# Kernel optimization log

Hardware: AMD Instinct MI355X
Metric: run time of the kernel (lower is better)

The kernel has to match this reference:

```python
import jax, jax.numpy as jnp
import numpy as np

B, N, C, H, T = 64, 4096, 768, 12, 10


def setup_inputs() -> dict:
    key = jax.random.key(0)
    kx, kq, kk, kv, kp = jax.random.split(key, 5)
    std = 0.02  # trunc_normal std from _init_weights
    return {
        "x": jax.random.normal(kx, (B, N, C), jnp.float32),
        "Wq": std * jax.random.normal(kq, (C, C), jnp.float32),
        "Wk": std * jax.random.normal(kk, (C, C), jnp.float32),
        "Wv": std * jax.random.normal(kv, (C, C), jnp.float32),
        "Wp": std * jax.random.normal(kp, (C, C), jnp.float32),
        "bp": jnp.zeros((C,), jnp.float32),
        "nb_task_tokens": T,
    }


def reference(x, Wq, Wk, Wv, Wp, bp, nb_task_tokens):
    Bq, Nq, Cq = x.shape
    d = Cq // H
    scale = d ** -0.5
    Tt = nb_task_tokens
    # q only from the first T (task) tokens; k, v from all N tokens
    q = (x[:, :Tt] @ Wq).reshape(Bq, Tt, H, d).transpose(0, 2, 1, 3) * scale  # [B,H,T,d]
    k = (x @ Wk).reshape(Bq, Nq, H, d).transpose(0, 2, 1, 3)                  # [B,H,N,d]
    v = (x @ Wv).reshape(Bq, Nq, H, d).transpose(0, 2, 1, 3)                  # [B,H,N,d]
    attn = jnp.einsum("bhtd,bhnd->bhtn", q, k)                                # [B,H,T,N]
    # mask: task token i may attend to itself and to all patch tokens (cols >= T),
    # but not to other task tokens
    rows = jnp.arange(Tt)[:, None]
    cols = jnp.arange(Nq)[None, :]
    allowed = (cols >= Tt) | (cols == rows)                                   # [T,N]
    attn = jnp.where(allowed, attn, -jnp.inf)
    attn = jax.nn.softmax(attn, axis=-1)
    x_cls = jnp.einsum("bhtn,bhnd->bhtd", attn, v)                            # [B,H,T,d]
    x_cls = x_cls.transpose(0, 2, 1, 3).reshape(Bq, Tt, Cq)
    x_cls = x_cls @ Wp + bp
    return (x_cls, attn, v)
```

## Files before the change

### kernel.cpp

```cpp
#include <hip/hip_runtime.h>

typedef __attribute__((ext_vector_type(8))) short short8;
typedef __attribute__((ext_vector_type(4))) short short4v;
typedef __attribute__((ext_vector_type(4))) float f32x4;

__device__ __forceinline__ unsigned short f2bf(float f) {
  union { float f; unsigned u; } v; v.f = f;
  unsigned r = v.u + 0x7FFFu + ((v.u >> 16) & 1u);
  return (unsigned short)(r >> 16);
}

__device__ __forceinline__ float bf2f(unsigned short h) {
  union { unsigned u; float f; } v; v.u = ((unsigned)h) << 16;
  return v.f;
}

__device__ __forceinline__ void gload16(const void* g, void* l) {
  __builtin_amdgcn_global_load_lds(
      (const __attribute__((address_space(1))) void*)g,
      (__attribute__((address_space(3))) void*)l, 16, 0, 0);
}

__global__ __launch_bounds__(256) void conv_x(const float* __restrict__ x,
                                              unsigned short* __restrict__ xb) {
  const long total = 25165824;
  long stride = (long)gridDim.x * 256;
  for (long u = blockIdx.x * 256 + threadIdx.x; u < total; u += stride) {
    const float* p = x + u * 8;
    float4 a = *(const float4*)p;
    float4 b = *(const float4*)(p + 4);
    short8 h;
    h[0] = (short)f2bf(a.x); h[1] = (short)f2bf(a.y);
    h[2] = (short)f2bf(a.z); h[3] = (short)f2bf(a.w);
    h[4] = (short)f2bf(b.x); h[5] = (short)f2bf(b.y);
    h[6] = (short)f2bf(b.z); h[7] = (short)f2bf(b.w);
    *(short8*)(xb + u * 8) = h;
  }
}

__global__ __launch_bounds__(256) void prep_w(const float* __restrict__ Wk,
                                              const float* __restrict__ Wv,
                                              unsigned short* __restrict__ Wt) {
  int idx = blockIdx.x * 256 + threadIdx.x;
  int n = idx / 768, k = idx - n * 768;
  float w = (n < 768) ? Wk[k * 768 + n] : Wv[k * 768 + (n - 768)];
  Wt[idx] = f2bf(w);
}

__global__ __launch_bounds__(256) void q_proj(const float* __restrict__ x,
                                              const float* __restrict__ Wq,
                                              unsigned short* __restrict__ q_ws) {
  int b = blockIdx.x, tid = threadIdx.x;
  __shared__ float xr[7680];
  const float* xp = x + (long)b * 4096 * 768;
  for (int i = tid; i < 7680; i += 256) xr[i] = xp[i];
  for (int i = tid; i < 12 * 6 * 64; i += 256) {
    int h = i / 384, rem = i - h * 384;
    int t = 10 + rem / 64, d = rem & 63;
    q_ws[(((long)(b * 12 + h) * 16 + t) << 6) + d] = 0;
  }
  __syncthreads();
  float acc[10][3];
#pragma unroll
  for (int t = 0; t < 10; ++t) { acc[t][0] = 0.f; acc[t][1] = 0.f; acc[t][2] = 0.f; }
  for (int k = 0; k < 768; ++k) {
    const float* wr = Wq + (long)k * 768;
    float w0 = wr[tid], w1 = wr[tid + 256], w2 = wr[tid + 512];
#pragma unroll
    for (int t = 0; t < 10; ++t) {
      float xv = xr[t * 768 + k];
      acc[t][0] += xv * w0; acc[t][1] += xv * w1; acc[t][2] += xv * w2;
    }
  }
#pragma unroll
  for (int t = 0; t < 10; ++t) {
#pragma unroll
    for (int j = 0; j < 3; ++j) {
      int c = tid + j * 256;
      int h = c >> 6, d = c & 63;
      q_ws[(((long)(b * 12 + h) * 16 + t) << 6) + d] = f2bf(acc[t][j] * 0.125f);
    }
  }
}

__global__ __launch_bounds__(512, 2) void gemm_kv8(const unsigned short* __restrict__ xb,
                                                   const unsigned short* __restrict__ Wt,
                                                   unsigned short* __restrict__ k_ws,
                                                   float* __restrict__ v_out) {
  __shared__ char smem[131072];
#define A0T ((unsigned short*)(smem))
#define B0T ((unsigned short*)(smem + 32768))
#define A1T ((unsigned short*)(smem + 65536))
#define B1T ((unsigned short*)(smem + 98304))

  int bid = blockIdx.x;
  int lb = (bid & 7) * 768 + (bid >> 3);
  int mt = lb / 6, nt = lb - mt * 6;
  long m0 = (long)mt * 256; int n0 = nt * 256;
  int tid = threadIdx.x, lane = tid & 63;
  int uw = __builtin_amdgcn_readfirstlane(tid >> 6);
  int wm = uw >> 2, wn = uw & 3;
  int r16 = lane & 15, gk = lane >> 4;

  const unsigned short* xs = xb + m0 * 768;
  const unsigned short* wp = Wt + (long)n0 * 768;

  int srow8 = lane >> 3;
  int sch = ((lane & 7) ^ (srow8 & 7)) << 3;
  const unsigned short* sA = xs + (long)(uw * 8 + srow8) * 768 + sch;
  const unsigned short* sB = wp + (long)(uw * 8 + srow8) * 768 + sch;

  int ck0 = ((gk ^ (r16 & 7)) << 3);
  int ck1 = (((4 + gk) ^ (r16 & 7)) << 3);
  int arb = (wm * 128 + r16) * 64;
  int brb = (wn * 64 + r16) * 64;

  f32x4 acc[8][4];
#pragma unroll
  for (int i = 0; i < 8; ++i)
#pragma unroll
    for (int j = 0; j < 4; ++j) acc[i][j] = (f32x4){0.f, 0.f, 0.f, 0.f};

#define SGA(AT, I, KO) gload16(sA + (long)(I) * 49152 + (KO), (AT) + ((I) * 64 + uw * 8) * 64)
#define SGB(BT, I, KO) gload16(sB + (long)(I) * 49152 + (KO), (BT) + ((I) * 64 + uw * 8) * 64)
#define WBND asm volatile("s_waitcnt vmcnt(0)\n\ts_barrier" ::: "memory")
#define PBAR __builtin_amdgcn_s_barrier()

#define BODY(AC, BC, AN, BN, KOS, DOST)                                         \
  {                                                                             \
    short8 fa[4][2], fb0[2][2], fb1[2][2];                                      \
    if (DOST) { SGA(AN, 0, KOS); SGA(AN, 1, KOS); SGB(BN, 0, KOS); SGB(BN, 1, KOS); } \
    _Pragma("unroll")                                                           \
    for (int mi = 0; mi < 4; ++mi) {                                            \
      fa[mi][0] = *(const short8*)&AC[arb + mi * 1024 + ck0];                   \
      fa[mi][1] = *(const short8*)&AC[arb + mi * 1024 + ck1];                   \
    }                                                                           \
    _Pragma("unroll")                                                           \
    for (int ni = 0; ni < 2; ++ni) {                                            \
      fb0[ni][0] = *(const short8*)&BC[brb + ni * 1024 + ck0];                  \
      fb0[ni][1] = *(const short8*)&BC[brb + ni * 1024 + ck1];                  \
    }                                                                           \
    PBAR;                                                                       \
    __builtin_amdgcn_s_setprio(1);                                              \
    _Pragma("unroll")                                                           \
    for (int mi = 0; mi < 4; ++mi)                                              \
      _Pragma("unroll")                                                         \
      for (int ni = 0; ni < 2; ++ni) {                                          \
        acc[mi][ni] = __builtin_amdgcn_mfma_f32_16x16x32_bf16(fa[mi][0], fb0[ni][0], acc[mi][ni], 0, 0, 0); \
        acc[mi][ni] = __builtin_amdgcn_mfma_f32_16x16x32_bf16(fa[mi][1], fb0[ni][1], acc[mi][ni], 0, 0, 0); \
      }                                                                         \
    __builtin_amdgcn_s_setprio(0);                                              \
    PBAR;                                                                       \
    if (DOST) { SGA(AN, 2, KOS); SGA(AN, 3, KOS); SGB(BN, 2, KOS); SGB(BN, 3, KOS); } \
    _Pragma("unroll")                                                           \
    for (int ni = 0; ni < 2; ++ni) {                                            \
      fb1[ni][0] = *(const short8*)&BC[brb + (ni + 2) * 1024 + ck0];            \
      fb1[ni][1] = *(const short8*)&BC[brb + (ni + 2) * 1024 + ck1];            \
    }                                                                           \
    PBAR;                                                                       \
    __builtin_amdgcn_s_setprio(1);                                              \
    _Pragma("unroll")                                                           \
    for (int mi = 0; mi < 4; ++mi)                                              \
      _Pragma("unroll")                                                         \
      for (int ni = 0; ni < 2; ++ni) {                                          \
        acc[mi][ni + 2] = __builtin_amdgcn_mfma_f32_16x16x32_bf16(fa[mi][0], fb1[ni][0], acc[mi][ni + 2], 0, 0, 0); \
        acc[mi][ni + 2] = __builtin_amdgcn_mfma_f32_16x16x32_bf16(fa[mi][1], fb1[ni][1], acc[mi][ni + 2], 0, 0, 0); \
      }                                                                         \
    __builtin_amdgcn_s_setprio(0);                                              \
    PBAR;                                                                       \
    _Pragma("unroll")                                                           \
    for (int mi = 0; mi < 4; ++mi) {                                            \
      fa[mi][0] = *(const short8*)&AC[arb + (mi + 4) * 1024 + ck0];             \
      fa[mi][1] = *(const short8*)&AC[arb + (mi + 4) * 1024 + ck1];             \
    }                                                                           \
    PBAR;                                                                       \
    __builtin_amdgcn_s_setprio(1);                                              \
    _Pragma("unroll")                                                           \
    for (int mi = 0; mi < 4; ++mi)                                              \
      _Pragma("unroll")                                                         \
      for (int ni = 0; ni < 2; ++ni) {                                          \
        acc[mi + 4][ni + 2] = __builtin_amdgcn_mfma_f32_16x16x32_bf16(fa[mi][0], fb1[ni][0], acc[mi + 4][ni + 2], 0, 0, 0); \
        acc[mi + 4][ni + 2] = __builtin_amdgcn_mfma_f32_16x16x32_bf16(fa[mi][1], fb1[ni][1], acc[mi + 4][ni + 2], 0, 0, 0); \
      }                                                                         \
    __builtin_amdgcn_s_setprio(0);                                              \
    PBAR;                                                                       \
    __builtin_amdgcn_s_setprio(1);                                              \
    _Pragma("unroll")                                                           \
    for (int mi = 0; mi < 4; ++mi)                                              \
      _Pragma("unroll")                                                         \
      for (int ni = 0; ni < 2; ++ni) {                                          \
        acc[mi + 4][ni] = __builtin_amdgcn_mfma_f32_16x16x32_bf16(fa[mi][0], fb0[ni][0], acc[mi + 4][ni], 0, 0, 0); \
        acc[mi + 4][ni] = __builtin_amdgcn_mfma_f32_16x16x32_bf16(fa[mi][1], fb0[ni][1], acc[mi + 4][ni], 0, 0, 0); \
      }                                                                         \
    __builtin_amdgcn_s_setprio(0);                                              \
  }

  SGA(A0T, 0, 0); SGA(A0T, 1, 0); SGA(A0T, 2, 0); SGA(A0T, 3, 0);
  SGB(B0T, 0, 0); SGB(B0T, 1, 0); SGB(B0T, 2, 0); SGB(B0T, 3, 0);
  WBND;

#pragma unroll 1
  for (int t = 0; t < 12; t += 2) {
    BODY(A0T, B0T, A1T, B1T, (t + 1) * 64, true);
    WBND;
    BODY(A1T, B1T, A0T, B0T, (t + 2) * 64, (t + 2) < 12);
    WBND;
  }
#undef BODY
#undef SGA
#undef SGB
#undef WBND
#undef PBAR

  float* scr = (float*)smem + uw * 1088;
  bool is_k = (n0 < 768);
  int h = (is_k ? (n0 >> 6) : ((n0 - 768) >> 6)) + wn;
  int bq = (int)(m0 >> 12);
  int nb = (int)(m0 & 4095) + wm * 128;

#pragma unroll
  for (int mi = 0; mi < 8; ++mi) {
#pragma unroll
    for (int ni = 0; ni < 4; ++ni)
#pragma unroll
      for (int r = 0; r < 4; ++r)
        scr[(gk * 4 + r) * 68 + ni * 16 + r16] = acc[mi][ni][r];
    int nbase = nb + mi * 16;
    if (is_k) {
#pragma unroll
      for (int p = 0; p < 2; ++p) {
        int row = p * 8 + (lane >> 3), d0 = (lane & 7) << 3;
        float4 aa = *(const float4*)&scr[row * 68 + d0];
        float4 bb = *(const float4*)&scr[row * 68 + d0 + 4];
        short8 hh;
        hh[0] = (short)f2bf(aa.x); hh[1] = (short)f2bf(aa.y);
        hh[2] = (short)f2bf(aa.z); hh[3] = (short)f2bf(aa.w);
        hh[4] = (short)f2bf(bb.x); hh[5] = (short)f2bf(bb.y);
        hh[6] = (short)f2bf(bb.z); hh[7] = (short)f2bf(bb.w);
        *(short8*)&k_ws[((long)(bq * 12 + h) * 4096 + nbase + row) * 64 + d0] = hh;
      }
    } else {
#pragma unroll
      for (int p = 0; p < 4; ++p) {
        int row = p * 4 + (lane >> 4), d0 = (lane & 15) << 2;
        float4 aa = *(const float4*)&scr[row * 68 + d0];
        *(float4*)&v_out[((long)(bq * 12 + h) * 4096 + nbase + row) * 64 + d0] = aa;
      }
    }
  }
#undef A0T
#undef B0T
#undef A1T
#undef B1T
}

__global__ __launch_bounds__(256) void gemm_kv(const float* __restrict__ x,
                                               const unsigned short* __restrict__ Wt,
                                               unsigned short* __restrict__ k_ws,
                                               float* __restrict__ v_out) {
  __shared__ char lds[32768];
  int bid = blockIdx.x;
  int lb = (bid & 7) * 3072 + (bid >> 3);
  int mt = lb / 12, nt = lb - mt * 12;
  long m0 = (long)mt * 128; int n0 = nt * 128;
  int tid = threadIdx.x, lane = tid & 63;
  int wid = tid >> 6, wm = wid >> 1, wn = wid & 1;
  int rlo = lane & 15, gk = lane >> 4;

  const float* xs = x + m0 * 768;
  const unsigned short* wp = Wt + (long)n0 * 768;

  int arow0 = tid >> 3, ak4 = (tid & 7) << 2;
  int bn = tid >> 1, bg = (tid & 1) << 1;

  f32x4 acc[4][4];
#pragma unroll
  for (int i = 0; i < 4; ++i)
#pragma unroll
    for (int j = 0; j < 4; ++j) acc[i][j] = (f32x4){0.f, 0.f, 0.f, 0.f};

  float4 fA[4]; short8 wB[2];
#pragma unroll
  for (int it = 0; it < 4; ++it) {
    int row = it * 32 + arow0;
    fA[it] = *(const float4*)(xs + (long)row * 768 + ak4);
  }
#pragma unroll
  for (int i = 0; i < 2; ++i)
    wB[i] = *(const short8*)(wp + (long)bn * 768 + (bg + i) * 8);
#pragma unroll
  for (int it = 0; it < 4; ++it) {
    int row = it * 32 + arow0;
    short4v h;
    h[0] = (short)f2bf(fA[it].x); h[1] = (short)f2bf(fA[it].y);
    h[2] = (short)f2bf(fA[it].z); h[3] = (short)f2bf(fA[it].w);
    *(short4v*)(lds + row * 64 + ((ak4 * 2) ^ (((row >> 1) & 3) << 4))) = h;
  }
#pragma unroll
  for (int i = 0; i < 2; ++i)
    *(short8*)(lds + 16384 + bn * 64 + (((bg + i) * 16) ^ (((bn >> 1) & 3) << 4))) = wB[i];
  __syncthreads();

#pragma unroll 2
  for (int ks = 0; ks < 24; ++ks) {
    char* Ab = lds + (ks & 1) * 8192;
    char* Bb = lds + 16384 + (ks & 1) * 8192;
    bool pf = (ks + 1 < 24);
    if (pf) {
#pragma unroll
      for (int it = 0; it < 4; ++it) {
        int row = it * 32 + arow0;
        fA[it] = *(const float4*)(xs + (long)row * 768 + (ks + 1) * 32 + ak4);
      }
#pragma unroll
      for (int i = 0; i < 2; ++i)
        wB[i] = *(const short8*)(wp + (long)bn * 768 + (ks + 1) * 32 + (bg + i) * 8);
    }
    short8 af[4], bfr[4];
#pragma unroll
    for (int mi = 0; mi < 4; ++mi) {
      int row = wm * 64 + mi * 16 + rlo;
      af[mi] = *(const short8*)(Ab + row * 64 + ((gk * 16) ^ (((row >> 1) & 3) << 4)));
    }
#pragma unroll
    for (int ni = 0; ni < 4; ++ni) {
      int n = wn * 64 + ni * 16 + rlo;
      bfr[ni] = *(const short8*)(Bb + n * 64 + ((gk * 16) ^ (((n >> 1) & 3) << 4)));
    }
#pragma unroll
    for (int mi = 0; mi < 4; ++mi)
#pragma unroll
      for (int ni = 0; ni < 4; ++ni)
        acc[mi][ni] = __builtin_amdgcn_mfma_f32_16x16x32_bf16(af[mi], bfr[ni], acc[mi][ni], 0, 0, 0);
    if (pf) {
      char* An = lds + ((ks + 1) & 1) * 8192;
      char* Bn = lds + 16384 + ((ks + 1) & 1) * 8192;
#pragma unroll
      for (int it = 0; it < 4; ++it) {
        int row = it * 32 + arow0;
        short4v h;
        h[0] = (short)f2bf(fA[it].x); h[1] = (short)f2bf(fA[it].y);
        h[2] = (short)f2bf(fA[it].z); h[3] = (short)f2bf(fA[it].w);
        *(short4v*)(An + row * 64 + ((ak4 * 2) ^ (((row >> 1) & 3) << 4))) = h;
      }
#pragma unroll
      for (int i = 0; i < 2; ++i)
        *(short8*)(Bn + bn * 64 + (((bg + i) * 16) ^ (((bn >> 1) & 3) << 4))) = wB[i];
    }
    __syncthreads();
  }

  bool is_k = (n0 < 768);
  int cb = is_k ? n0 : n0 - 768;
#pragma unroll
  for (int ni = 0; ni < 4; ++ni) {
    int cc = cb + wn * 64 + ni * 16 + rlo;
    int h = cc >> 6, d = cc & 63;
#pragma unroll
    for (int mi = 0; mi < 4; ++mi) {
#pragma unroll
      for (int r = 0; r < 4; ++r) {
        long m = m0 + wm * 64 + mi * 16 + gk * 4 + r;
        int b = (int)(m >> 12), n = (int)(m & 4095);
        long off = ((long)(b * 12 + h) * 4096 + n) * 64 + d;
        float val = acc[mi][ni][r];
        if (is_k) k_ws[off] = f2bf(val);
        else      v_out[off] = val;
      }
    }
  }
}

__global__ __launch_bounds__(512) void attn_fused3(const unsigned short* __restrict__ k_ws,
                                                   const unsigned short* __restrict__ q_ws,
                                                   const float* __restrict__ v_glob,
                                                   float* __restrict__ attn_out,
                                                   float* __restrict__ preproj) {
  __shared__ char blob[115712];
  unsigned short* pbuf = (unsigned short*)blob;
  float* part = (float*)(blob + 81920);
  float* redm = (float*)(blob + 114688);
  float* rowmax16 = redm + 128;
  float* rowinv16 = rowmax16 + 16;

  int tid = threadIdx.x, lane = tid & 63, w = tid >> 6;
  int bh = blockIdx.x;
  int r16 = lane & 15, gk = lane >> 4;
  int trc = (r16 < 10) ? r16 : 9;
  int nW = w << 9;

  const unsigned short* kp = k_ws + (long)bh * (4096 * 64);
  const unsigned short* qp = q_ws + (long)bh * 1024;
  float* sraw = attn_out + (long)bh * 40960;
  const float* vp = v_glob + (long)bh * (4096 * 64);

  short8 qf0 = *(const short8*)(qp + r16 * 64 + gk * 8);
  short8 qf1 = *(const short8*)(qp + r16 * 64 + 32 + gk * 8);

  char* pbw = (char*)pbuf + w * 10240 + r16 * 1024;
  int swz = (r16 & 7) << 4;

  float pmax = -3.0e38f;
#pragma unroll 4
  for (int ch = 0; ch < 32; ++ch) {
    int n0 = nW + (ch << 4);
    short8 kf0 = *(const short8*)(kp + (long)(n0 + r16) * 64 + gk * 8);
    short8 kf1 = *(const short8*)(kp + (long)(n0 + r16) * 64 + 32 + gk * 8);
    f32x4 d4 = (f32x4){0.f, 0.f, 0.f, 0.f};
    d4 = __builtin_amdgcn_mfma_f32_16x16x32_bf16(kf0, qf0, d4, 0, 0, 0);
    d4 = __builtin_amdgcn_mfma_f32_16x16x32_bf16(kf1, qf1, d4, 0, 0, 0);
#pragma unroll
    for (int r = 0; r < 4; ++r) {
      int n = n0 + gk * 4 + r;
      float v = d4[r];
      if (n < 10 && n != r16) v = -1e30f;
      d4[r] = v;
      pmax = fmaxf(pmax, v);
    }
    if (r16 < 10) {
      short4v h4;
      h4[0] = (short)f2bf(d4[0]); h4[1] = (short)f2bf(d4[1]);
      h4[2] = (short)f2bf(d4[2]); h4[3] = (short)f2bf(d4[3]);
      *(short4v*)(pbw + ((ch * 32 + gk * 8) ^ swz)) = h4;
    }
  }
  pmax = fmaxf(pmax, __shfl_xor(pmax, 16));
  pmax = fmaxf(pmax, __shfl_xor(pmax, 32));
  if (lane < 16) redm[w * 16 + lane] = pmax;
  __syncthreads();
  if (tid < 16) {
    float m = redm[tid];
#pragma unroll
    for (int i = 1; i < 8; ++i) m = fmaxf(m, redm[i * 16 + tid]);
    rowmax16[tid] = m;
  }
  __syncthreads();

  float mx = rowmax16[trc];
  char* pbr = (char*)pbuf + w * 10240 + trc * 1024;
  int swr = (trc & 7) << 4;
  float psum = 0.f;
#pragma unroll 4
  for (int i = 0; i < 16; ++i) {
    short8 sv = *(const short8*)(pbr + ((i * 64 + gk * 16) ^ swr));
#pragma unroll
    for (int j = 0; j < 8; ++j) psum += __expf(bf2f((unsigned short)sv[j]) - mx);
  }
  psum += __shfl_xor(psum, 16);
  psum += __shfl_xor(psum, 32);
  if (lane < 16) redm[w * 16 + lane] = psum;
  __syncthreads();
  if (tid < 16) {
    float t = 0.f;
#pragma unroll
    for (int i = 0; i < 8; ++i) t += redm[i * 16 + tid];
    rowinv16[tid] = 1.0f / t;
  }
  __syncthreads();
  float inv = rowinv16[trc];

  if (r16 < 10) {
#pragma unroll 4
    for (int i = 0; i < 16; ++i) {
      short8 sv = *(const short8*)(pbw + ((i * 64 + gk * 16) ^ swz));
      float4 o0, o1;
      o0.x = __expf(bf2f((unsigned short)sv[0]) - mx) * inv;
      o0.y = __expf(bf2f((unsigned short)sv[1]) - mx) * inv;
      o0.z = __expf(bf2f((unsigned short)sv[2]) - mx) * inv;
      o0.w = __expf(bf2f((unsigned short)sv[3]) - mx) * inv;
      o1.x = __expf(bf2f((unsigned short)sv[4]) - mx) * inv;
      o1.y = __expf(bf2f((unsigned short)sv[5]) - mx) * inv;
      o1.z = __expf(bf2f((unsigned short)sv[6]) - mx) * inv;
      o1.w = __expf(bf2f((unsigned short)sv[7]) - mx) * inv;
      float* gp = sraw + r16 * 4096 + nW + i * 32 + gk * 8;
      *(float4*)gp = o0;
      *(float4*)(gp + 4) = o1;
    }
  }

  f32x4 pacc[4];
#pragma unroll
  for (int dc = 0; dc < 4; ++dc) pacc[dc] = (f32x4){0.f, 0.f, 0.f, 0.f};
#pragma unroll 2
  for (int ks = 0; ks < 16; ++ks) {
    short8 raw = *(const short8*)(pbr + ((ks * 64 + gk * 16) ^ swr));
    short8 pa;
#pragma unroll
    for (int j = 0; j < 8; ++j)
      pa[j] = (short)f2bf(__expf(bf2f((unsigned short)raw[j]) - mx) * inv);
    const float* vbase = vp + (long)(nW + ks * 32 + gk * 8) * 64 + r16;
#pragma unroll
    for (int dc = 0; dc < 4; ++dc) {
      short8 vb;
      const float* vrow = vbase + dc * 16;
#pragma unroll
      for (int j = 0; j < 8; ++j) vb[j] = (short)f2bf(vrow[j * 64]);
      pacc[dc] = __builtin_amdgcn_mfma_f32_16x16x32_bf16(pa, vb, pacc[dc], 0, 0, 0);
    }
  }
#pragma unroll
  for (int dc = 0; dc < 4; ++dc)
#pragma unroll
    for (int r = 0; r < 4; ++r)
      part[w * 1024 + dc * 256 + (gk * 4 + r) * 16 + r16] = pacc[dc][r];
  __syncthreads();

  int b = bh / 12, h = bh - b * 12;
  for (int idx = tid; idx < 640; idx += 512) {
    int tt = idx >> 6, d = idx & 63;
    int dc = d >> 4, dl = d & 15;
    float sum = 0.f;
#pragma unroll
    for (int i = 0; i < 8; ++i) sum += part[i * 1024 + dc * 256 + tt * 16 + dl];
    preproj[((long)b * 10 + tt) * 768 + h * 64 + d] = sum;
  }
}

__global__ __launch_bounds__(256) void proj_out_k(const float* __restrict__ preproj,
                                                  const float* __restrict__ Wp,
                                                  const float* __restrict__ bp,
                                                  float* __restrict__ out0) {
  int b = blockIdx.x, tid = threadIdx.x;
  __shared__ float xr[7680];
  const float* pp = preproj + (long)b * 7680;
  for (int i = tid; i < 7680; i += 256) xr[i] = pp[i];
  __syncthreads();
  float acc[10][3];
#pragma unroll
  for (int t = 0; t < 10; ++t) { acc[t][0] = 0.f; acc[t][1] = 0.f; acc[t][2] = 0.f; }
  for (int k = 0; k < 768; ++k) {
    const float* wr = Wp + (long)k * 768;
    float w0 = wr[tid], w1 = wr[tid + 256], w2 = wr[tid + 512];
#pragma unroll
    for (int t = 0; t < 10; ++t) {
      float xv = xr[t * 768 + k];
      acc[t][0] += xv * w0; acc[t][1] += xv * w1; acc[t][2] += xv * w2;
    }
  }
  float b0 = bp[tid], b1 = bp[tid + 256], b2 = bp[tid + 512];
  float* op = out0 + (long)b * 7680;
#pragma unroll
  for (int t = 0; t < 10; ++t) {
    op[t * 768 + tid]       = acc[t][0] + b0;
    op[t * 768 + tid + 256] = acc[t][1] + b1;
    op[t * 768 + tid + 512] = acc[t][2] + b2;
  }
}

extern "C" void kernel_launch(void* const* d_in, const int* in_sizes, int n_in,
                              void* d_out, int out_size, void* d_ws, size_t ws_size,
                              hipStream_t stream) {
  (void)in_sizes; (void)n_in; (void)out_size;
  const float* x  = (const float*)d_in[0];
  const float* Wq = (const float*)d_in[1];
  const float* Wk = (const float*)d_in[2];
  const float* Wv = (const float*)d_in[3];
  const float* Wp = (const float*)d_in[4];
  const float* bp = (const float*)d_in[5];

  float* out      = (float*)d_out;
  float* attn_out = out + 491520;
  float* v_out    = out + 31948800;

  char* ws = (char*)d_ws;
  const size_t NEED_BIG = 811204608;

  if (ws_size >= NEED_BIG) {
    unsigned short* x_bf16 = (unsigned short*)(ws);
    unsigned short* k_ws = (unsigned short*)(ws + 402653184);
    unsigned short* q_ws = (unsigned short*)(ws + 805306368);
    unsigned short* Wt   = (unsigned short*)(ws + 806879232);
    float* preproj       = (float*)(ws + 809238528);

    conv_x<<<dim3(2048), dim3(256), 0, stream>>>(x, x_bf16);
    prep_w<<<dim3(4608), dim3(256), 0, stream>>>(Wk, Wv, Wt);
    q_proj<<<dim3(64), dim3(256), 0, stream>>>(x, Wq, q_ws);
    gemm_kv8<<<dim3(6144), dim3(512), 0, stream>>>(x_bf16, Wt, k_ws, v_out);
    attn_fused3<<<dim3(768), dim3(512), 0, stream>>>(k_ws, q_ws, v_out, attn_out, preproj);
    proj_out_k<<<dim3(64), dim3(256), 0, stream>>>(preproj, Wp, bp, out);
  } else {
    unsigned short* k_ws = (unsigned short*)(ws);
    unsigned short* q_ws = (unsigned short*)(ws + 402653184);
    unsigned short* Wt   = (unsigned short*)(ws + 404226048);
    float* preproj       = (float*)(ws + 406585344);

    prep_w<<<dim3(4608), dim3(256), 0, stream>>>(Wk, Wv, Wt);
    q_proj<<<dim3(64), dim3(256), 0, stream>>>(x, Wq, q_ws);
    gemm_kv<<<dim3(24576), dim3(256), 0, stream>>>(x, Wt, k_ws, v_out);
    attn_fused3<<<dim3(768), dim3(512), 0, stream>>>(k_ws, q_ws, v_out, attn_out, preproj);
    proj_out_k<<<dim3(64), dim3(256), 0, stream>>>(preproj, Wp, bp, out);
  }
}
```

Measured before the change: 1.491 ms.

## Emit transposed bf16 V from the KV GEMM and read it in attention

The KV GEMM epilogue now also writes a bf16 copy of V transposed to [B,H,d,N] in a new workspace buffer. The attention kernel then loads V B-operand fragments as contiguous 16-byte vectors instead of gathering eight strided fp32 values per fragment and converting them. This removes the strided fp32 gather and conversion in the PV MFMA loop. In exchange it adds an extra bf16 V write and scratch traffic in the GEMM epilogue, and it needs a larger workspace; if the workspace is smaller, the older path is used instead.

Result: slower. 1.567 ms (+5.0%).

```diff
diff --git a/kernel.cpp b/kernel.cpp
--- a/kernel.cpp
+++ b/kernel.cpp
@@ -82,44 +82,6 @@
     }
   }
 }
-
-__global__ __launch_bounds__(512, 2) void gemm_kv8(const unsigned short* __restrict__ xb,
-                                                   const unsigned short* __restrict__ Wt,
-                                                   unsigned short* __restrict__ k_ws,
-                                                   float* __restrict__ v_out) {
-  __shared__ char smem[131072];
-#define A0T ((unsigned short*)(smem))
-#define B0T ((unsigned short*)(smem + 32768))
-#define A1T ((unsigned short*)(smem + 65536))
-#define B1T ((unsigned short*)(smem + 98304))
-
-  int bid = blockIdx.x;
-  int lb = (bid & 7) * 768 + (bid >> 3);
-  int mt = lb / 6, nt = lb - mt * 6;
-  long m0 = (long)mt * 256; int n0 = nt * 256;
-  int tid = threadIdx.x, lane = tid & 63;
-  int uw = __builtin_amdgcn_readfirstlane(tid >> 6);
-  int wm = uw >> 2, wn = uw & 3;
-  int r16 = lane & 15, gk = lane >> 4;
-
-  const unsigned short* xs = xb + m0 * 768;
-  const unsigned short* wp = Wt + (long)n0 * 768;
-
-  int srow8 = lane >> 3;
-  int sch = ((lane & 7) ^ (srow8 & 7)) << 3;
-  const unsigned short* sA = xs + (long)(uw * 8 + srow8) * 768 + sch;
-  const unsigned short* sB = wp + (long)(uw * 8 + srow8) * 768 + sch;
-
-  int ck0 = ((gk ^ (r16 & 7)) << 3);
-  int ck1 = (((4 + gk) ^ (r16 & 7)) << 3);
-  int arb = (wm * 128 + r16) * 64;
-  int brb = (wn * 64 + r16) * 64;
-
-  f32x4 acc[8][4];
-#pragma unroll
-  for (int i = 0; i < 8; ++i)
-#pragma unroll
-    for (int j = 0; j < 4; ++j) acc[i][j] = (f32x4){0.f, 0.f, 0.f, 0.f};
 
 #define SGA(AT, I, KO) gload16(sA + (long)(I) * 49152 + (KO), (AT) + ((I) * 64 + uw * 8) * 64)
 #define SGB(BT, I, KO) gload16(sB + (long)(I) * 49152 + (KO), (BT) + ((I) * 64 + uw * 8) * 64)
@@ -195,29 +157,145 @@
     __builtin_amdgcn_s_setprio(0);                                              \
   }
 
-  SGA(A0T, 0, 0); SGA(A0T, 1, 0); SGA(A0T, 2, 0); SGA(A0T, 3, 0);
-  SGB(B0T, 0, 0); SGB(B0T, 1, 0); SGB(B0T, 2, 0); SGB(B0T, 3, 0);
-  WBND;
-
-#pragma unroll 1
-  for (int t = 0; t < 12; t += 2) {
-    BODY(A0T, B0T, A1T, B1T, (t + 1) * 64, true);
-    WBND;
-    BODY(A1T, B1T, A0T, B0T, (t + 2) * 64, (t + 2) < 12);
-    WBND;
-  }
-#undef BODY
-#undef SGA
-#undef SGB
-#undef WBND
-#undef PBAR
+#define GEMM_PROLOGUE                                                           \
+  int bid = blockIdx.x;                                                         \
+  int lb = (bid & 7) * 768 + (bid >> 3);                                        \
+  int mt = lb / 6;                                                              \
+  int nt = lb - mt * 6;                                                         \
+  long m0 = (long)mt * 256;                                                     \
+  int n0 = nt * 256;                                                            \
+  int tid = threadIdx.x;                                                        \
+  int lane = tid & 63;                                                          \
+  int uw = __builtin_amdgcn_readfirstlane(tid >> 6);                            \
+  int wm = uw >> 2;                                                             \
+  int wn = uw & 3;                                                              \
+  int r16 = lane & 15;                                                          \
+  int gk = lane >> 4;                                                           \
+  const unsigned short* xs = xb + m0 * 768;                                     \
+  const unsigned short* wp = Wt + (long)n0 * 768;                               \
+  int srow8 = lane >> 3;                                                        \
+  int sch = ((lane & 7) ^ (srow8 & 7)) << 3;                                    \
+  const unsigned short* sA = xs + (long)(uw * 8 + srow8) * 768 + sch;           \
+  const unsigned short* sB = wp + (long)(uw * 8 + srow8) * 768 + sch;           \
+  int ck0 = ((gk ^ (r16 & 7)) << 3);                                            \
+  int ck1 = (((4 + gk) ^ (r16 & 7)) << 3);                                      \
+  int arb = (wm * 128 + r16) * 64;                                              \
+  int brb = (wn * 64 + r16) * 64;                                               \
+  f32x4 acc[8][4];                                                              \
+  _Pragma("unroll")                                                             \
+  for (int i = 0; i < 8; ++i)                                                   \
+    _Pragma("unroll")                                                           \
+    for (int j = 0; j < 4; ++j) acc[i][j] = (f32x4){0.f, 0.f, 0.f, 0.f};        \
+  SGA(A0T, 0, 0); SGA(A0T, 1, 0); SGA(A0T, 2, 0); SGA(A0T, 3, 0);               \
+  SGB(B0T, 0, 0); SGB(B0T, 1, 0); SGB(B0T, 2, 0); SGB(B0T, 3, 0);               \
+  WBND;                                                                         \
+  _Pragma("unroll 1")                                                           \
+  for (int t = 0; t < 12; t += 2) {                                             \
+    BODY(A0T, B0T, A1T, B1T, (t + 1) * 64, true);                               \
+    WBND;                                                                       \
+    BODY(A1T, B1T, A0T, B0T, (t + 2) * 64, (t + 2) < 12);                       \
+    WBND;                                                                       \
+  }
+
+__global__ __launch_bounds__(512, 2) void gemm_kv9(const unsigned short* __restrict__ xb,
+                                                   const unsigned short* __restrict__ Wt,
+                                                   unsigned short* __restrict__ k_ws,
+                                                   float* __restrict__ v_out,
+                                                   unsigned short* __restrict__ vt) {
+  __shared__ char smem[131072];
+  unsigned short* A0T = (unsigned short*)(smem);
+  unsigned short* B0T = (unsigned short*)(smem + 32768);
+  unsigned short* A1T = (unsigned short*)(smem + 65536);
+  unsigned short* B1T = (unsigned short*)(smem + 98304);
+  GEMM_PROLOGUE
+
+  float* scr0 = (float*)smem + uw * 2176;
+  float* scr1 = scr0 + 1088;
+  bool is_k = (n0 < 768);
+  int h = (is_k ? (n0 >> 6) : ((n0 - 768) >> 6)) + wn;
+  int bq = (int)(m0 >> 12);
+  int nb = (int)(m0 & 4095) + wm * 128;
+
+  if (is_k) {
+#pragma unroll
+    for (int mi = 0; mi < 8; ++mi) {
+#pragma unroll
+      for (int ni = 0; ni < 4; ++ni)
+#pragma unroll
+        for (int r = 0; r < 4; ++r)
+          scr0[(gk * 4 + r) * 68 + ni * 16 + r16] = acc[mi][ni][r];
+      int nbase = nb + mi * 16;
+#pragma unroll
+      for (int p = 0; p < 2; ++p) {
+        int row = p * 8 + (lane >> 3);
+        int d0 = (lane & 7) << 3;
+        float4 aa = *(const float4*)&scr0[row * 68 + d0];
+        float4 bb = *(const float4*)&scr0[row * 68 + d0 + 4];
+        short8 hh;
+        hh[0] = (short)f2bf(aa.x); hh[1] = (short)f2bf(aa.y);
+        hh[2] = (short)f2bf(aa.z); hh[3] = (short)f2bf(aa.w);
+        hh[4] = (short)f2bf(bb.x); hh[5] = (short)f2bf(bb.y);
+        hh[6] = (short)f2bf(bb.z); hh[7] = (short)f2bf(bb.w);
+        *(short8*)&k_ws[((long)(bq * 12 + h) * 4096 + nbase + row) * 64 + d0] = hh;
+      }
+    }
+  } else {
+    unsigned short* vTp = vt + ((long)(bq * 12 + h) * 64) * 4096;
+#pragma unroll
+    for (int mp = 0; mp < 4; ++mp) {
+      int nbase = nb + mp * 32;
+#pragma unroll
+      for (int ni = 0; ni < 4; ++ni)
+#pragma unroll
+        for (int r = 0; r < 4; ++r) {
+          scr0[(gk * 4 + r) * 68 + ni * 16 + r16] = acc[mp * 2][ni][r];
+          scr1[(gk * 4 + r) * 68 + ni * 16 + r16] = acc[mp * 2 + 1][ni][r];
+        }
+#pragma unroll
+      for (int p = 0; p < 4; ++p) {
+        int row = p * 4 + (lane >> 4);
+        int d0 = (lane & 15) << 2;
+        float4 a0 = *(const float4*)&scr0[row * 68 + d0];
+        *(float4*)&v_out[((long)(bq * 12 + h) * 4096 + nbase + row) * 64 + d0] = a0;
+        float4 a1 = *(const float4*)&scr1[row * 68 + d0];
+        *(float4*)&v_out[((long)(bq * 12 + h) * 4096 + nbase + 16 + row) * 64 + d0] = a1;
+      }
+      short8 w0;
+      short8 w1;
+      short8 w2;
+      short8 w3;
+#pragma unroll
+      for (int i = 0; i < 8; ++i) {
+        w0[i] = (short)f2bf(scr0[i * 68 + lane]);
+        w1[i] = (short)f2bf(scr0[(i + 8) * 68 + lane]);
+        w2[i] = (short)f2bf(scr1[i * 68 + lane]);
+        w3[i] = (short)f2bf(scr1[(i + 8) * 68 + lane]);
+      }
+      unsigned short* vrow = vTp + (long)lane * 4096 + nbase;
+      *(short8*)(vrow)      = w0;
+      *(short8*)(vrow + 8)  = w1;
+      *(short8*)(vrow + 16) = w2;
+      *(short8*)(vrow + 24) = w3;
+    }
+  }
+}
+
+__global__ __launch_bounds__(512, 2) void gemm_kv8(const unsigned short* __restrict__ xb,
+                                                   const unsigned short* __restrict__ Wt,
+                                                   unsigned short* __restrict__ k_ws,
+                                                   float* __restrict__ v_out) {
+  __shared__ char smem[131072];
+  unsigned short* A0T = (unsigned short*)(smem);
+  unsigned short* B0T = (unsigned short*)(smem + 32768);
+  unsigned short* A1T = (unsigned short*)(smem + 65536);
+  unsigned short* B1T = (unsigned short*)(smem + 98304);
+  GEMM_PROLOGUE
 
   float* scr = (float*)smem + uw * 1088;
   bool is_k = (n0 < 768);
   int h = (is_k ? (n0 >> 6) : ((n0 - 768) >> 6)) + wn;
   int bq = (int)(m0 >> 12);
   int nb = (int)(m0 & 4095) + wm * 128;
-
 #pragma unroll
   for (int mi = 0; mi < 8; ++mi) {
 #pragma unroll
@@ -229,7 +307,8 @@
     if (is_k) {
 #pragma unroll
       for (int p = 0; p < 2; ++p) {
-        int row = p * 8 + (lane >> 3), d0 = (lane & 7) << 3;
+        int row = p * 8 + (lane >> 3);
+        int d0 = (lane & 7) << 3;
         float4 aa = *(const float4*)&scr[row * 68 + d0];
         float4 bb = *(const float4*)&scr[row * 68 + d0 + 4];
         short8 hh;
@@ -242,17 +321,21 @@
     } else {
 #pragma unroll
       for (int p = 0; p < 4; ++p) {
-        int row = p * 4 + (lane >> 4), d0 = (lane & 15) << 2;
+        int row = p * 4 + (lane >> 4);
+        int d0 = (lane & 15) << 2;
         float4 aa = *(const float4*)&scr[row * 68 + d0];
         *(float4*)&v_out[((long)(bq * 12 + h) * 4096 + nbase + row) * 64 + d0] = aa;
       }
     }
   }
-#undef A0T
-#undef B0T
-#undef A1T
-#undef B1T
-}
+}
+
+#undef GEMM_PROLOGUE
+#undef BODY
+#undef SGA
+#undef SGB
+#undef WBND
+#undef PBAR
 
 __global__ __launch_bounds__(256) void gemm_kv(const float* __restrict__ x,
                                                const unsigned short* __restrict__ Wt,
@@ -371,9 +454,9 @@
   }
 }
 
-__global__ __launch_bounds__(512) void attn_fused3(const unsigned short* __restrict__ k_ws,
+__global__ __launch_bounds__(512) void attn_fused4(const unsigned short* __restrict__ k_ws,
                                                    const unsigned short* __restrict__ q_ws,
-                                                   const float* __restrict__ v_glob,
+                                                   const unsigned short* __restrict__ vt,
                                                    float* __restrict__ attn_out,
                                                    float* __restrict__ preproj) {
   __shared__ char blob[115712];
@@ -392,7 +475,7 @@
   const unsigned short* kp = k_ws + (long)bh * (4096 * 64);
   const unsigned short* qp = q_ws + (long)bh * 1024;
   float* sraw = attn_out + (long)bh * 40960;
-  const float* vp = v_glob + (long)bh * (4096 * 64);
+  const unsigned short* vtp = vt + (long)bh * (64 * 4096);
 
   short8 qf0 = *(const short8*)(qp + r16 * 64 + gk * 8);
   short8 qf1 = *(const short8*)(qp + r16 * 64 + 32 + gk * 8);
@@ -488,6 +571,148 @@
 #pragma unroll
     for (int j = 0; j < 8; ++j)
       pa[j] = (short)f2bf(__expf(bf2f((unsigned short)raw[j]) - mx) * inv);
+    int nbb = nW + ks * 32 + gk * 8;
+#pragma unroll
+    for (int dc = 0; dc < 4; ++dc) {
+      short8 vb = *(const short8*)&vtp[(long)(dc * 16 + r16) * 4096 + nbb];
+      pacc[dc] = __builtin_amdgcn_mfma_f32_16x16x32_bf16(pa, vb, pacc[dc], 0, 0, 0);
+    }
+  }
+#pragma unroll
+  for (int dc = 0; dc < 4; ++dc)
+#pragma unroll
+    for (int r = 0; r < 4; ++r)
+      part[w * 1024 + dc * 256 + (gk * 4 + r) * 16 + r16] = pacc[dc][r];
+  __syncthreads();
+
+  int b = bh / 12, h = bh - b * 12;
+  for (int idx = tid; idx < 640; idx += 512) {
+    int tt = idx >> 6, d = idx & 63;
+    int dc = d >> 4, dl = d & 15;
+    float sum = 0.f;
+#pragma unroll
+    for (int i = 0; i < 8; ++i) sum += part[i * 1024 + dc * 256 + tt * 16 + dl];
+    preproj[((long)b * 10 + tt) * 768 + h * 64 + d] = sum;
+  }
+}
+
+__global__ __launch_bounds__(512) void attn_fused3(const unsigned short* __restrict__ k_ws,
+                                                   const unsigned short* __restrict__ q_ws,
+                                                   const float* __restrict__ v_glob,
+                                                   float* __restrict__ attn_out,
+                                                   float* __restrict__ preproj) {
+  __shared__ char blob[115712];
+  unsigned short* pbuf = (unsigned short*)blob;
+  float* part = (float*)(blob + 81920);
+  float* redm = (float*)(blob + 114688);
+  float* rowmax16 = redm + 128;
+  float* rowinv16 = rowmax16 + 16;
+
+  int tid = threadIdx.x, lane = tid & 63, w = tid >> 6;
+  int bh = blockIdx.x;
+  int r16 = lane & 15, gk = lane >> 4;
+  int trc = (r16 < 10) ? r16 : 9;
+  int nW = w << 9;
+
+  const unsigned short* kp = k_ws + (long)bh * (4096 * 64);
+  const unsigned short* qp = q_ws + (long)bh * 1024;
+  float* sraw = attn_out + (long)bh * 40960;
+  const float* vp = v_glob + (long)bh * (4096 * 64);
+
+  short8 qf0 = *(const short8*)(qp + r16 * 64 + gk * 8);
+  short8 qf1 = *(const short8*)(qp + r16 * 64 + 32 + gk * 8);
+
+  char* pbw = (char*)pbuf + w * 10240 + r16 * 1024;
+  int swz = (r16 & 7) << 4;
+
+  float pmax = -3.0e38f;
+#pragma unroll 4
+  for (int ch = 0; ch < 32; ++ch) {
+    int n0 = nW + (ch << 4);
+    short8 kf0 = *(const short8*)(kp + (long)(n0 + r16) * 64 + gk * 8);
+    short8 kf1 = *(const short8*)(kp + (long)(n0 + r16) * 64 + 32 + gk * 8);
+    f32x4 d4 = (f32x4){0.f, 0.f, 0.f, 0.f};
+    d4 = __builtin_amdgcn_mfma_f32_16x16x32_bf16(kf0, qf0, d4, 0, 0, 0);
+    d4 = __builtin_amdgcn_mfma_f32_16x16x32_bf16(kf1, qf1, d4, 0, 0, 0);
+#pragma unroll
+    for (int r = 0; r < 4; ++r) {
+      int n = n0 + gk * 4 + r;
+      float v = d4[r];
+      if (n < 10 && n != r16) v = -1e30f;
+      d4[r] = v;
+      pmax = fmaxf(pmax, v);
+    }
+    if (r16 < 10) {
+      short4v h4;
+      h4[0] = (short)f2bf(d4[0]); h4[1] = (short)f2bf(d4[1]);
+      h4[2] = (short)f2bf(d4[2]); h4[3] = (short)f2bf(d4[3]);
+      *(short4v*)(pbw + ((ch * 32 + gk * 8) ^ swz)) = h4;
+    }
+  }
+  pmax = fmaxf(pmax, __shfl_xor(pmax, 16));
+  pmax = fmaxf(pmax, __shfl_xor(pmax, 32));
+  if (lane < 16) redm[w * 16 + lane] = pmax;
+  __syncthreads();
+  if (tid < 16) {
+    float m = redm[tid];
+#pragma unroll
+    for (int i = 1; i < 8; ++i) m = fmaxf(m, redm[i * 16 + tid]);
+    rowmax16[tid] = m;
+  }
+  __syncthreads();
+
+  float mx = rowmax16[trc];
+  char* pbr = (char*)pbuf + w * 10240 + trc * 1024;
+  int swr = (trc & 7) << 4;
+  float psum = 0.f;
+#pragma unroll 4
+  for (int i = 0; i < 16; ++i) {
+    short8 sv = *(const short8*)(pbr + ((i * 64 + gk * 16) ^ swr));
+#pragma unroll
+    for (int j = 0; j < 8; ++j) psum += __expf(bf2f((unsigned short)sv[j]) - mx);
+  }
+  psum += __shfl_xor(psum, 16);
+  psum += __shfl_xor(psum, 32);
+  if (lane < 16) redm[w * 16 + lane] = psum;
+  __syncthreads();
+  if (tid < 16) {
+    float t = 0.f;
+#pragma unroll
+    for (int i = 0; i < 8; ++i) t += redm[i * 16 + tid];
+    rowinv16[tid] = 1.0f / t;
+  }
+  __syncthreads();
+  float inv = rowinv16[trc];
+
+  if (r16 < 10) {
+#pragma unroll 4
+    for (int i = 0; i < 16; ++i) {
+      short8 sv = *(const short8*)(pbw + ((i * 64 + gk * 16) ^ swz));
+      float4 o0, o1;
+      o0.x = __expf(bf2f((unsigned short)sv[0]) - mx) * inv;
+      o0.y = __expf(bf2f((unsigned short)sv[1]) - mx) * inv;
+      o0.z = __expf(bf2f((unsigned short)sv[2]) - mx) * inv;
+      o0.w = __expf(bf2f((unsigned short)sv[3]) - mx) * inv;
+      o1.x = __expf(bf2f((unsigned short)sv[4]) - mx) * inv;
+      o1.y = __expf(bf2f((unsigned short)sv[5]) - mx) * inv;
+      o1.z = __expf(bf2f((unsigned short)sv[6]) - mx) * inv;
+      o1.w = __expf(bf2f((unsigned short)sv[7]) - mx) * inv;
+      float* gp = sraw + r16 * 4096 + nW + i * 32 + gk * 8;
+      *(float4*)gp = o0;
+      *(float4*)(gp + 4) = o1;
+    }
+  }
+
+  f32x4 pacc[4];
+#pragma unroll
+  for (int dc = 0; dc < 4; ++dc) pacc[dc] = (f32x4){0.f, 0.f, 0.f, 0.f};
+#pragma unroll 2
+  for (int ks = 0; ks < 16; ++ks) {
+    short8 raw = *(const short8*)(pbr + ((ks * 64 + gk * 16) ^ swr));
+    short8 pa;
+#pragma unroll
+    for (int j = 0; j < 8; ++j)
+      pa[j] = (short)f2bf(__expf(bf2f((unsigned short)raw[j]) - mx) * inv);
     const float* vbase = vp + (long)(nW + ks * 32 + gk * 8) * 64 + r16;
 #pragma unroll
     for (int dc = 0; dc < 4; ++dc) {
@@ -563,14 +788,29 @@
   float* v_out    = out + 31948800;
 
   char* ws = (char*)d_ws;
+  const size_t NEED_VT  = 1213857792;
   const size_t NEED_BIG = 811204608;
 
-  if (ws_size >= NEED_BIG) {
+  if (ws_size >= NEED_VT) {
     unsigned short* x_bf16 = (unsigned short*)(ws);
-    unsigned short* k_ws = (unsigned short*)(ws + 402653184);
-    unsigned short* q_ws = (unsigned short*)(ws + 805306368);
-    unsigned short* Wt   = (unsigned short*)(ws + 806879232);
-    float* preproj       = (float*)(ws + 809238528);
+    unsigned short* k_ws   = (unsigned short*)(ws + 402653184);
+    unsigned short* vt_ws  = (unsigned short*)(ws + 805306368);
+    unsigned short* q_ws   = (unsigned short*)(ws + 1207959552);
+    unsigned short* Wt     = (unsigned short*)(ws + 1209532416);
+    float* preproj         = (float*)(ws + 1211891712);
+
+    conv_x<<<dim3(2048), dim3(256), 0, stream>>>(x, x_bf16);
+    prep_w<<<dim3(4608), dim3(256), 0, stream>>>(Wk, Wv, Wt);
+    q_proj<<<dim3(64), dim3(256), 0, stream>>>(x, Wq, q_ws);
+    gemm_kv9<<<dim3(6144), dim3(512), 0, stream>>>(x_bf16, Wt, k_ws, v_out, vt_ws);
+    attn_fused4<<<dim3(768), dim3(512), 0, stream>>>(k_ws, q_ws, vt_ws, attn_out, preproj);
+    proj_out_k<<<dim3(64), dim3(256), 0, stream>>>(preproj, Wp, bp, out);
+  } else if (ws_size >= NEED_BIG) {
+    unsigned short* x_bf16 = (unsigned short*)(ws);
+    unsigned short* k_ws   = (unsigned short*)(ws + 402653184);
+    unsigned short* q_ws   = (unsigned short*)(ws + 805306368);
+    unsigned short* Wt     = (unsigned short*)(ws + 806879232);
+    float* preproj         = (float*)(ws + 809238528);
 
     conv_x<<<dim3(2048), dim3(256), 0, stream>>>(x, x_bf16);
     prep_w<<<dim3(4608), dim3(256), 0, stream>>>(Wk, Wv, Wt);
```
